# Optimization experiments

Hardware: AMD Instinct MI355X
Metric: run time of the kernel (lower is better)

## Reference

```python
import jax, jax.numpy as jnp
import numpy as np

N_QUBITS = 20
W_MUL = (2.0 ** 0.5) * (5.0 ** -0.5)  # he_std = gain * 5**-0.5, use_wscale=True, lrmul=1

_C = jnp.complex64
X = jnp.array([[0, 1], [1, 0]], dtype=_C)
Y = jnp.array([[0, -1j], [1j, 0]], dtype=_C)
Z = jnp.array([[1, 0], [0, -1]], dtype=_C)
I2 = jnp.eye(2, dtype=_C)
I4 = jnp.eye(4, dtype=_C)
XX = jnp.kron(X, X)
YY = jnp.kron(Y, Y)
ZZ = jnp.kron(Z, Z)


def _rot(theta, pauli, ident):
    # exp(-i * theta/2 * P) = cos(theta/2) I - i sin(theta/2) P
    a = theta * 0.5
    return jnp.cos(a) * ident - (1j * jnp.sin(a)) * pauli


def _apply_1q(state, g, w):
    # state: [batch] + [2]*n ; contract gate input index with qubit axis w
    s = jnp.tensordot(g, state, axes=((1,), (w + 1,)))
    return jnp.moveaxis(s, 0, w + 1)


def _apply_2q(state, g4, w0, w1):
    g = g4.reshape(2, 2, 2, 2)  # (out0, out1, in0, in1)
    s = jnp.tensordot(g, state, axes=((2, 3), (w0 + 1, w1 + 1)))
    return jnp.moveaxis(s, (0, 1), (w0 + 1, w1 + 1))


def _xyz_layer(psi, params, n):
    # params: [3n]; rx, ry, rz on each wire
    for q in range(n):
        psi = _apply_1q(psi, _rot(params[3 * q], X, I2), q)
        psi = _apply_1q(psi, _rot(params[3 * q + 1], Y, I2), q)
        psi = _apply_1q(psi, _rot(params[3 * q + 2], Z, I2), q)
    return psi


def _circuit(psi, w, n):
    psi = _xyz_layer(psi, w[: 3 * n], n)
    for q in range(n - 1):
        i = 3 * n + 3 * q
        psi = _apply_2q(psi, _rot(w[i], XX, I4), q, q + 1)
        psi = _apply_2q(psi, _rot(w[i + 1], YY, I4), q, q + 1)
        psi = _apply_2q(psi, _rot(w[i + 2], ZZ, I4), q, q + 1)
    psi = _xyz_layer(psi, w[6 * n - 3 :], n)
    return psi


def setup_inputs() -> dict:
    key = jax.random.key(0)
    k1, k2 = jax.random.split(key)
    n = N_QUBITS
    dim = 1 << n
    batch = 4
    x = jax.random.normal(k1, (batch, 1, dim), dtype=jnp.float32)
    weight = jax.random.uniform(k2, (9 * n - 3,), dtype=jnp.float32, minval=0.0, maxval=2.0 * np.pi)
    return {"x": x, "weight": weight, "dimA": 10}


def reference(x, weight, dimA):
    n = N_QUBITS
    batch = x.shape[0]
    w = weight * W_MUL
    psi = x.astype(_C).reshape((batch,) + (2,) * n)  # MPS tensor [b, 2, ..., 2]
    psi = _circuit(psi, w, n)
    dimB = n - dimA
    # partial trace of |psi><psi| over the first dimB qubits (most-significant axes):
    # reduced[a, c] = sum_t psi[t, a] * conj(psi[t, c])  -- never materialize the full DM
    psi = psi.reshape(batch, 1 << dimB, 1 << dimA)
    rdm = jnp.einsum('bta,btc->bac', psi, psi.conj())
    # return real/imag stacked on last axis (real-valued representation of complex DM)
    return jnp.stack([rdm.real, rdm.imag], axis=-1)
```

## Files before the change

### kernel.cpp

```cpp
#include <hip/hip_runtime.h>
#include <hip/hip_bf16.h>

#define N_Q    20
#define DIM    (1 << N_Q)
#define BATCH  4
#define NGATES 19
#define L2OFF  117
#define GSTRIDE 32

typedef float2 c32;
typedef __attribute__((ext_vector_type(2))) float fv2;
typedef __attribute__((ext_vector_type(8))) short short8;
typedef __attribute__((ext_vector_type(4))) float f32x4;
typedef __attribute__((ext_vector_type(4))) unsigned int u32x4;

__device__ __forceinline__ c32 cmul(c32 a, c32 b) {
    return make_float2(fmaf(a.x, b.x, -a.y * b.y), fmaf(a.x, b.y, a.y * b.x));
}
__device__ __forceinline__ c32 cmadd(c32 acc, c32 a, c32 b) {
    acc.x = fmaf(a.x, b.x, fmaf(-a.y, b.y, acc.x));
    acc.y = fmaf(a.x, b.y, fmaf(a.y, b.x, acc.y));
    return acc;
}
__device__ __forceinline__ unsigned short f2bf(float f) {
    union { float f; unsigned u; } v; v.f = f;
    unsigned r = v.u + 0x7FFFu + ((v.u >> 16) & 1u);
    return (unsigned short)(r >> 16);
}
__device__ __forceinline__ unsigned pack_bf2(float re, float im) {
    return (unsigned)f2bf(re) | ((unsigned)f2bf(im) << 16);
}
__device__ __forceinline__ fv2 unpack_bf2(unsigned w) {
    union { unsigned u; float f; } lo, hi;
    lo.u = (w & 0xFFFFu) << 16;
    hi.u = w & 0xFFFF0000u;
    return (fv2){lo.f, hi.f};
}
__device__ __forceinline__ void gll16(const void* g, void* l) {
    __builtin_amdgcn_global_load_lds((const __attribute__((address_space(1))) void*)g,
                                     (__attribute__((address_space(3))) void*)l, 16, 0, 0);
}

__device__ void mm2(const c32 A[2][2], const c32 B[2][2], c32 C[2][2]) {
    for (int i = 0; i < 2; i++)
        for (int j = 0; j < 2; j++) {
            c32 s = make_float2(0.f, 0.f);
            for (int k = 0; k < 2; k++) s = cmadd(s, A[i][k], B[k][j]);
            C[i][j] = s;
        }
}
__device__ void mm4(const c32 A[4][4], const c32 B[4][4], c32 C[4][4]) {
    for (int i = 0; i < 4; i++)
        for (int j = 0; j < 4; j++) {
            c32 s = make_float2(0.f, 0.f);
            for (int k = 0; k < 4; k++) s = cmadd(s, A[i][k], B[k][j]);
            C[i][j] = s;
        }
}
__device__ void single_u(const float* w, int base, c32 U[2][2]) {
    const float WM = 0.63245553203367586640f;
    float hx = w[base] * WM * 0.5f, hy = w[base + 1] * WM * 0.5f, hz = w[base + 2] * WM * 0.5f;
    float cx = cosf(hx), sx = sinf(hx);
    float cy = cosf(hy), sy = sinf(hy);
    float cz = cosf(hz), sz = sinf(hz);
    c32 RX[2][2] = {{{cx, 0.f}, {0.f, -sx}}, {{0.f, -sx}, {cx, 0.f}}};
    c32 RY[2][2] = {{{cy, 0.f}, {-sy, 0.f}}, {{sy, 0.f}, {cy, 0.f}}};
    c32 RZ[2][2] = {{{cz, -sz}, {0.f, 0.f}}, {{0.f, 0.f}, {cz, sz}}};
    c32 T[2][2];
    mm2(RY, RX, T);
    mm2(RZ, T, U);
}
__device__ void kron22(const c32 A[2][2], const c32 B[2][2], c32 K[4][4]) {
    for (int i = 0; i < 2; i++)
        for (int j = 0; j < 2; j++)
            for (int k = 0; k < 2; k++)
                for (int l = 0; l < 2; l++)
                    K[i * 2 + j][k * 2 + l] = cmul(A[i][k], B[j][l]);
}

__global__ void build_gates(const float* __restrict__ w, c32* __restrict__ G) {
    int q = threadIdx.x;
    if (q >= NGATES) return;
    const float WM = 0.63245553203367586640f;
    float hx = w[60 + 3 * q] * WM * 0.5f;
    float hy = w[61 + 3 * q] * WM * 0.5f;
    float hz = w[62 + 3 * q] * WM * 0.5f;
    float cx = cosf(hx), sx = sinf(hx);
    float cy = cosf(hy), sy = sinf(hy);
    float cz = cosf(hz), sz = sinf(hz);
    c32 RXX[4][4], RYY[4][4], RZZ[4][4];
    for (int i = 0; i < 4; i++)
        for (int j = 0; j < 4; j++) {
            RXX[i][j] = make_float2(0.f, 0.f);
            RYY[i][j] = make_float2(0.f, 0.f);
            RZZ[i][j] = make_float2(0.f, 0.f);
        }
    for (int i = 0; i < 4; i++) {
        RXX[i][i]     = make_float2(cx, 0.f);
        RXX[i][3 - i] = make_float2(0.f, -sx);
        RYY[i][i]     = make_float2(cy, 0.f);
    }
    RYY[0][3] = make_float2(0.f,  sy);
    RYY[1][2] = make_float2(0.f, -sy);
    RYY[2][1] = make_float2(0.f, -sy);
    RYY[3][0] = make_float2(0.f,  sy);
    RZZ[0][0] = make_float2(cz, -sz);
    RZZ[1][1] = make_float2(cz,  sz);
    RZZ[2][2] = make_float2(cz,  sz);
    RZZ[3][3] = make_float2(cz, -sz);
    c32 T[4][4], M[4][4];
    mm4(RYY, RXX, T);
    mm4(RZZ, T, M);

    c32 I2m[2][2] = {{{1.f, 0.f}, {0.f, 0.f}}, {{0.f, 0.f}, {1.f, 0.f}}};
    c32 Ua[2][2], Ub[2][2], Pre[4][4], Post[4][4];
    if (q == 0) {
        single_u(w, 0, Ua);
        single_u(w, 3, Ub);
        kron22(Ua, Ub, Pre);
    } else {
        single_u(w, 3 * (q + 1), Ub);
        kron22(I2m, Ub, Pre);
    }
    if (q == NGATES - 1) {
        single_u(w, L2OFF + 3 * 18, Ua);
        single_u(w, L2OFF + 3 * 19, Ub);
        kron22(Ua, Ub, Post);
    } else {
        single_u(w, L2OFF + 3 * q, Ua);
        kron22(Ua, I2m, Post);
    }
    c32 T2[4][4], Gq[4][4];
    mm4(M, Pre, T2);
    mm4(Post, T2, Gq);
    for (int i = 0; i < 4; i++)
        for (int j = 0; j < 4; j++) {
            c32 g = Gq[i][j];
            G[q * GSTRIDE + i * 4 + j]      = g;
            G[q * GSTRIDE + 16 + i * 4 + j] = make_float2(-g.y, g.x);
        }
}

__device__ __forceinline__ void apply4pk(const fv2 g[16], const fv2 gs[16],
                                         fv2& x0, fv2& x1, fv2& x2, fv2& x3) {
    fv2 a0 = (fv2)(x0[0]), b0 = (fv2)(x0[1]);
    fv2 a1 = (fv2)(x1[0]), b1 = (fv2)(x1[1]);
    fv2 a2 = (fv2)(x2[0]), b2 = (fv2)(x2[1]);
    fv2 a3 = (fv2)(x3[0]), b3 = (fv2)(x3[1]);
    fv2 r0 = a0 * g[0];  r0 += b0 * gs[0];  r0 += a1 * g[1];  r0 += b1 * gs[1];
    r0 += a2 * g[2];     r0 += b2 * gs[2];  r0 += a3 * g[3];  r0 += b3 * gs[3];
    fv2 r1 = a0 * g[4];  r1 += b0 * gs[4];  r1 += a1 * g[5];  r1 += b1 * gs[5];
    r1 += a2 * g[6];     r1 += b2 * gs[6];  r1 += a3 * g[7];  r1 += b3 * gs[7];
    fv2 r2 = a0 * g[8];  r2 += b0 * gs[8];  r2 += a1 * g[9];  r2 += b1 * gs[9];
    r2 += a2 * g[10];    r2 += b2 * gs[10]; r2 += a3 * g[11]; r2 += b3 * gs[11];
    fv2 r3 = a0 * g[12]; r3 += b0 * gs[12]; r3 += a1 * g[13]; r3 += b1 * gs[13];
    r3 += a2 * g[14];    r3 += b2 * gs[14]; r3 += a3 * g[15]; r3 += b3 * gs[15];
    x0 = r0; x1 = r1; x2 = r2; x3 = r3;
}
__device__ __forceinline__ void load_gate2(const fv2* __restrict__ gp, fv2 g[16], fv2 gs[16]) {
#pragma unroll
    for (int k = 0; k < 16; k++) { g[k] = gp[k]; gs[k] = gp[16 + k]; }
}
template <int LO>
__device__ __forceinline__ void gate_on32(fv2 v[32], const fv2 g[16], const fv2 gs[16]) {
#pragma unroll
    for (int m = 0; m < 8; ++m) {
        const int j0 = ((m >> LO) << (LO + 2)) | (m & ((1 << LO) - 1));
        const int s = 1 << LO;
        apply4pk(g, gs, v[j0], v[j0 + s], v[j0 + 2 * s], v[j0 + 3 * s]);
    }
}
template <int LO>
__device__ __forceinline__ void gate_on16(fv2* v, const fv2 g[16], const fv2 gs[16]) {
#pragma unroll
    for (int m = 0; m < 4; ++m) {
        const int j0 = ((m >> LO) << (LO + 2)) | (m & ((1 << LO) - 1));
        const int s = 1 << LO;
        apply4pk(g, gs, v[j0], v[j0 + s], v[j0 + 2 * s], v[j0 + 3 * s]);
    }
}

#define SIDX(l) ((l) ^ ((((l) >> 5) & 15)))

__global__ __launch_bounds__(256) void pass_a2(const float* __restrict__ x,
                                               unsigned* __restrict__ psiB,
                                               const c32* __restrict__ Gall) {
    __shared__ __align__(16) char smem[65536];
    float* xs = (float*)smem;
    fv2* s = (fv2*)smem;
    const fv2* Gf = (const fv2*)Gall;
    int b = blockIdx.x >> 7;
    int c0 = (blockIdx.x & 127) << 5;
    const float* xp = x + ((size_t)b << 20) + c0;
    unsigned* ppb = psiB + ((size_t)b << 20) + c0;
    int t = threadIdx.x;
#pragma unroll
    for (int i = 0; i < 8; ++i) {
        int f4 = t + (i << 8);
        int row = f4 >> 3, sl = f4 & 7;
        float4 v = *reinterpret_cast<const float4*>(xp + (size_t)row * 4096 + sl * 4);
        reinterpret_cast<float4*>(xs)[row * 8 + (sl ^ (row & 7))] = v;
    }
    __syncthreads();
    int col = t & 31, rlow = t >> 5;
    fv2 v[32], g[16], gs[16];
#pragma unroll
    for (int j = 0; j < 32; ++j) {
        int row = (j << 3) | rlow;
        float re = xs[row * 32 + ((((col >> 2) ^ (row & 7)) << 2) | (col & 3))];
        v[j] = (fv2){re, 0.f};
    }
    __syncthreads();
    load_gate2(Gf + 0 * GSTRIDE, g, gs);  gate_on32<3>(v, g, gs);
    load_gate2(Gf + 1 * GSTRIDE, g, gs);  gate_on32<2>(v, g, gs);
    load_gate2(Gf + 2 * GSTRIDE, g, gs);  gate_on32<1>(v, g, gs);
    load_gate2(Gf + 3 * GSTRIDE, g, gs);  gate_on32<0>(v, g, gs);
#pragma unroll
    for (int j = 0; j < 32; ++j) {
        int l = ((((j << 3) | rlow) << 5)) | col;
        s[SIDX(l)] = v[j];
    }
    __syncthreads();
    int rhi = t >> 5;
#pragma unroll
    for (int rtop = 0; rtop < 2; ++rtop)
#pragma unroll
        for (int j = 0; j < 16; ++j) {
            int row = (rtop << 7) | (rhi << 4) | j;
            int l = (row << 5) | col;
            v[rtop * 16 + j] = s[SIDX(l)];
        }
    load_gate2(Gf + 4 * GSTRIDE, g, gs);  gate_on16<2>(v, g, gs);  gate_on16<2>(v + 16, g, gs);
    load_gate2(Gf + 5 * GSTRIDE, g, gs);  gate_on16<1>(v, g, gs);  gate_on16<1>(v + 16, g, gs);
    load_gate2(Gf + 6 * GSTRIDE, g, gs);  gate_on16<0>(v, g, gs);  gate_on16<0>(v + 16, g, gs);
#pragma unroll
    for (int rtop = 0; rtop < 2; ++rtop)
#pragma unroll
        for (int j = 0; j < 16; ++j) {
            int row = (rtop << 7) | (rhi << 4) | j;
            fv2 val = v[rtop * 16 + j];
            ppb[(size_t)row * 4096 + col] = pack_bf2(val[0], val[1]);
        }
}

__global__ __launch_bounds__(256) void pass_b2(const unsigned* __restrict__ psiB,
                                               unsigned short* __restrict__ Brt,
                                               unsigned short* __restrict__ Bit,
                                               const c32* __restrict__ Gall) {
    __shared__ fv2 s[8192];
    const fv2* Gf = (const fv2*)Gall;
    int b = blockIdx.x >> 7;
    int chunk = blockIdx.x & 127;
    const unsigned* ppb = psiB + ((size_t)b << 20) + ((size_t)chunk << 13);
    int t = threadIdx.x;
    fv2 v[32], g[16], gs[16];
#pragma unroll
    for (int j = 0; j < 32; ++j) v[j] = unpack_bf2(ppb[(j << 8) | t]);
    load_gate2(Gf + 7 * GSTRIDE, g, gs);   gate_on32<3>(v, g, gs);
    load_gate2(Gf + 8 * GSTRIDE, g, gs);   gate_on32<2>(v, g, gs);
    load_gate2(Gf + 9 * GSTRIDE, g, gs);   gate_on32<1>(v, g, gs);
    load_gate2(Gf + 10 * GSTRIDE, g, gs);  gate_on32<0>(v, g, gs);
#pragma unroll
    for (int j = 0; j < 32; ++j) { int l = (j << 8) | t; s[SIDX(l)] = v[j]; }
    __syncthreads();
    int hi2 = (t >> 4) << 9, lo2 = t & 15;
#pragma unroll
    for (int j = 0; j < 32; ++j) { int l = hi2 | (j << 4) | lo2; v[j] = s[SIDX(l)]; }
    load_gate2(Gf + 11 * GSTRIDE, g, gs);  gate_on32<3>(v, g, gs);
    load_gate2(Gf + 12 * GSTRIDE, g, gs);  gate_on32<2>(v, g, gs);
    load_gate2(Gf + 13 * GSTRIDE, g, gs);  gate_on32<1>(v, g, gs);
    load_gate2(Gf + 14 * GSTRIDE, g, gs);  gate_on32<0>(v, g, gs);
    __syncthreads();
#pragma unroll
    for (int j = 0; j < 32; ++j) { int l = hi2 | (j << 4) | lo2; s[SIDX(l)] = v[j]; }
    __syncthreads();
#pragma unroll
    for (int j = 0; j < 32; ++j) { int l = (t << 5) | j; v[j] = s[SIDX(l)]; }
    load_gate2(Gf + 15 * GSTRIDE, g, gs);  gate_on32<3>(v, g, gs);
    load_gate2(Gf + 16 * GSTRIDE, g, gs);  gate_on32<2>(v, g, gs);
    load_gate2(Gf + 17 * GSTRIDE, g, gs);  gate_on32<1>(v, g, gs);
    load_gate2(Gf + 18 * GSTRIDE, g, gs);  gate_on32<0>(v, g, gs);
    size_t off = ((size_t)b << 20) + ((size_t)chunk << 13) + ((size_t)t << 5);
#pragma unroll
    for (int p = 0; p < 4; ++p) {
        unsigned short rr[8], ri[8];
#pragma unroll
        for (int i = 0; i < 8; ++i) {
            rr[i] = f2bf(v[8 * p + i][0]);
            ri[i] = f2bf(v[8 * p + i][1]);
        }
        *reinterpret_cast<float4*>(Brt + off + 8 * p) = *reinterpret_cast<float4*>(rr);
        *reinterpret_cast<float4*>(Bit + off + 8 * p) = *reinterpret_cast<float4*>(ri);
    }
}

__global__ __launch_bounds__(256) void bt_t(const unsigned short* __restrict__ Brt,
                                            const unsigned short* __restrict__ Bit,
                                            unsigned short* __restrict__ Art,
                                            unsigned short* __restrict__ Ait) {
    __shared__ unsigned lds32[64 * 66];
    int b  = blockIdx.z;
    int t0 = blockIdx.x * 64;
    int a0 = blockIdx.y * 64;
    size_t gb = (size_t)b << 20;
#pragma unroll
    for (int h = 0; h < 2; ++h) {
        int p = threadIdx.x + h * 256;
        int r = p >> 3, cq = p & 7;
        size_t src = gb + (size_t)(t0 + r) * 1024 + a0 + cq * 8;
        float4 fr = *reinterpret_cast<const float4*>(Brt + src);
        float4 fi = *reinterpret_cast<const float4*>(Bit + src);
        const unsigned short* ur = reinterpret_cast<const unsigned short*>(&fr);
        const unsigned short* ui = reinterpret_cast<const unsigned short*>(&fi);
#pragma unroll
        for (int i = 0; i < 8; ++i)
            lds32[r * 66 + cq * 8 + i] = (unsigned)ur[i] | ((unsigned)ui[i] << 16);
    }
    __syncthreads();
#pragma unroll
    for (int h = 0; h < 2; ++h) {
        int q = threadIdx.x + h * 256;
        int a = q >> 3, tq = q & 7;
        unsigned short rr[8], ri[8];
#pragma unroll
        for (int i = 0; i < 8; ++i) {
            unsigned w = lds32[(tq * 8 + i) * 66 + a];
            rr[i] = (unsigned short)(w & 0xFFFF);
            ri[i] = (unsigned short)(w >> 16);
        }
        size_t dst = gb + (size_t)(a0 + a) * 1024 + t0 + tq * 8;
        *reinterpret_cast<float4*>(Art + dst) = *reinterpret_cast<float4*>(rr);
        *reinterpret_cast<float4*>(Ait + dst) = *reinterpret_cast<float4*>(ri);
    }
}

__global__ __launch_bounds__(512) void gram_mfma5c(const unsigned short* __restrict__ Art,
                                                   const unsigned short* __restrict__ Ait,
                                                   float2* __restrict__ out) {
    __shared__ __align__(16) unsigned short lds[2][4][8192];
    int hw = blockIdx.x;
    int virt = (hw & 7) * 18 + (hw >> 3);
    int b = virt / 36;
    int rem = virt - b * 36;
    int ia = 0;
    while (rem >= 8 - ia) { rem -= 8 - ia; ++ia; }
    int ic = ia + rem;
    int a0 = ia * 128, c0 = ic * 128;
    int tid = threadIdx.x;
    int lane = tid & 63, w = tid >> 6;
    int wm = w & 3, wn = w >> 2;
    int arr = w >> 1, half = w & 1;
    const unsigned short* sp = (arr & 1) ? Ait : Art;
    int prow = (arr < 2) ? a0 : c0;
    int srow = lane >> 3, sslot = lane & 7;
    size_t gb = (size_t)b << 20;

    f32x4 accRe[2][4], accIm[2][4];
#pragma unroll
    for (int m = 0; m < 2; m++)
#pragma unroll
        for (int n = 0; n < 4; n++) { accRe[m][n] = (f32x4)0.f; accIm[m][n] = (f32x4)0.f; }

#define STAGE5(KT, BUF)                                                                   \
    {                                                                                     \
        _Pragma("unroll")                                                                 \
        for (int i = 0; i < 8; ++i) {                                                     \
            int r = (half << 6) | (i << 3) | srow;                                        \
            int sl = sslot ^ srow;                                                        \
            const unsigned short* gp = sp + gb + ((size_t)(prow + r) << 10) + (KT) * 64 + sl * 8; \
            gll16(gp, &lds[BUF][arr][((half << 6) | (i << 3)) * 64 + lane * 8]);          \
        }                                                                                 \
    }

    STAGE5(0, 0);
    for (int kt = 0; kt < 16; ++kt) {
        int cur = kt & 1;
        asm volatile("s_waitcnt vmcnt(0)" ::: "memory");
        __builtin_amdgcn_s_barrier();
        __builtin_amdgcn_sched_barrier(0);
        if (kt < 15) STAGE5(kt + 1, cur ^ 1);
        __builtin_amdgcn_s_setprio(1);
#pragma unroll
        for (int kk = 0; kk < 2; ++kk) {
            int sbase = kk * 4 + (lane >> 4);
            short8 am[2][2], bn[4][2];
#pragma unroll
            for (int m = 0; m < 2; m++) {
                int r = wm * 32 + m * 16 + (lane & 15);
                int off = r * 64 + ((sbase ^ (r & 7)) << 3);
                am[m][0] = *reinterpret_cast<const short8*>(&lds[cur][0][off]);
                am[m][1] = *reinterpret_cast<const short8*>(&lds[cur][1][off]);
            }
#pragma unroll
            for (int n = 0; n < 4; n++) {
                int r = wn * 64 + n * 16 + (lane & 15);
                int off = r * 64 + ((sbase ^ (r & 7)) << 3);
                bn[n][0] = *reinterpret_cast<const short8*>(&lds[cur][2][off]);
                bn[n][1] = *reinterpret_cast<const short8*>(&lds[cur][3][off]);
            }
#pragma unroll
            for (int m = 0; m < 2; m++) {
                u32x4 tn = *reinterpret_cast<u32x4*>(&am[m][0]) ^ 0x80008000u;
                short8 arn = *reinterpret_cast<short8*>(&tn);
#pragma unroll
                for (int n = 0; n < 4; n++) {
                    accRe[m][n] = __builtin_amdgcn_mfma_f32_16x16x32_bf16(am[m][0], bn[n][0], accRe[m][n], 0, 0, 0);
                    accRe[m][n] = __builtin_amdgcn_mfma_f32_16x16x32_bf16(am[m][1], bn[n][1], accRe[m][n], 0, 0, 0);
                    accIm[m][n] = __builtin_amdgcn_mfma_f32_16x16x32_bf16(am[m][1], bn[n][0], accIm[m][n], 0, 0, 0);
                    accIm[m][n] = __builtin_amdgcn_mfma_f32_16x16x32_bf16(arn,      bn[n][1], accIm[m][n], 0, 0, 0);
                }
            }
        }
        __builtin_amdgcn_s_setprio(0);
        asm volatile("s_waitcnt lgkmcnt(0)" ::: "memory");
        __builtin_amdgcn_sched_barrier(0);
    }
#undef STAGE5
    size_t ob = gb;
#pragma unroll
    for (int m = 0; m < 2; m++)
#pragma unroll
        for (int n = 0; n < 4; n++)
#pragma unroll
            for (int r = 0; r < 4; r++) {
                int a = a0 + wm * 32 + m * 16 + (lane >> 4) * 4 + r;
                int c = c0 + wn * 64 + n * 16 + (lane & 15);
                out[ob + ((size_t)a << 10) + c] = make_float2(accRe[m][n][r], accIm[m][n][r]);
            }
    if (ia != ic) {
        float2* mlds = reinterpret_cast<float2*>(&lds[0][0][0]);
#pragma unroll
        for (int h = 0; h < 2; ++h) {
            __syncthreads();
            if (wn == h) {
#pragma unroll
                for (int m = 0; m < 2; m++)
#pragma unroll
                    for (int n = 0; n < 4; n++)
#pragma unroll
                        for (int r = 0; r < 4; r++) {
                            int a_l = wm * 32 + m * 16 + (lane >> 4) * 4 + r;
                            int c_l = n * 16 + (lane & 15);
                            mlds[c_l * 131 + a_l] = make_float2(accRe[m][n][r], -accIm[m][n][r]);
                        }
            }
            __syncthreads();
#pragma unroll
            for (int i = 0; i < 16; ++i) {
                int p = tid + (i << 9);
                int row = p >> 7, col = p & 127;
                out[ob + ((size_t)(c0 + h * 64 + row) << 10) + a0 + col] = mlds[row * 131 + col];
            }
        }
    }
}

extern "C" void kernel_launch(void* const* d_in, const int* in_sizes, int n_in,
                              void* d_out, int out_size, void* d_ws, size_t ws_size,
                              hipStream_t stream) {
    const float* x = (const float*)d_in[0];
    const float* weight = (const float*)d_in[1];
    const size_t psiBytes = (size_t)BATCH * DIM * sizeof(unsigned);
    unsigned* psiB = (unsigned*)d_ws;
    c32* G = (c32*)((char*)d_ws + psiBytes);
    unsigned short* Brt = (unsigned short*)((char*)d_ws + psiBytes + 65536);
    unsigned short* Bit = Brt + (size_t)BATCH * DIM;
    unsigned short* Art = Bit + (size_t)BATCH * DIM;
    unsigned short* Ait = Art + (size_t)BATCH * DIM;

    build_gates<<<1, 64, 0, stream>>>(weight, G);
    pass_a2<<<BATCH * 128, 256, 0, stream>>>(x, psiB, G);
    pass_b2<<<BATCH * 128, 256, 0, stream>>>(psiB, Brt, Bit, G);
    bt_t<<<dim3(16, 16, BATCH), 256, 0, stream>>>(Brt, Bit, Art, Ait);
    gram_mfma5c<<<144, 512, 0, stream>>>(Art, Ait, (float2*)d_out);
}
```

Measured before the change: 94.38 us.

## Fuse transpose into pass_b2 epilogue and drop separate bt_t kernel

The final transpose that built the a-major bf16 planes is folded into pass_b2: after the last gate stage, each block stages its 8 t-rows by 1024 a-columns chunk in LDS with an XOR swizzle and writes 16-byte segments directly into the transposed Art/Ait layout. This removes one kernel launch and a full global round trip of the intermediate bf16 buffers. In exchange, the writes are now 16-byte pieces strided by 2 KB per row, which may coalesce less well, and pass_b2 gains an extra LDS pass and barrier.

```diff
diff --git a/kernel.cpp b/kernel.cpp
--- a/kernel.cpp
+++ b/kernel.cpp
@@ -181,6 +181,7 @@
 }
 
 #define SIDX(l) ((l) ^ ((((l) >> 5) & 15)))
+#define TIDX(a, tl) (((a) << 3) | ((tl) ^ (((a) >> 5) & 7)))
 
 __global__ __launch_bounds__(256) void pass_a2(const float* __restrict__ x,
                                                unsigned* __restrict__ psiB,
@@ -244,8 +245,8 @@
 }
 
 __global__ __launch_bounds__(256) void pass_b2(const unsigned* __restrict__ psiB,
-                                               unsigned short* __restrict__ Brt,
-                                               unsigned short* __restrict__ Bit,
+                                               unsigned short* __restrict__ Art,
+                                               unsigned short* __restrict__ Ait,
                                                const c32* __restrict__ Gall) {
     __shared__ fv2 s[8192];
     const fv2* Gf = (const fv2*)Gall;
@@ -280,57 +281,34 @@
     load_gate2(Gf + 16 * GSTRIDE, g, gs);  gate_on32<2>(v, g, gs);
     load_gate2(Gf + 17 * GSTRIDE, g, gs);  gate_on32<1>(v, g, gs);
     load_gate2(Gf + 18 * GSTRIDE, g, gs);  gate_on32<0>(v, g, gs);
-    size_t off = ((size_t)b << 20) + ((size_t)chunk << 13) + ((size_t)t << 5);
-#pragma unroll
-    for (int p = 0; p < 4; ++p) {
-        unsigned short rr[8], ri[8];
-#pragma unroll
-        for (int i = 0; i < 8; ++i) {
-            rr[i] = f2bf(v[8 * p + i][0]);
-            ri[i] = f2bf(v[8 * p + i][1]);
-        }
-        *reinterpret_cast<float4*>(Brt + off + 8 * p) = *reinterpret_cast<float4*>(rr);
-        *reinterpret_cast<float4*>(Bit + off + 8 * p) = *reinterpret_cast<float4*>(ri);
-    }
-}
-
-__global__ __launch_bounds__(256) void bt_t(const unsigned short* __restrict__ Brt,
-                                            const unsigned short* __restrict__ Bit,
-                                            unsigned short* __restrict__ Art,
-                                            unsigned short* __restrict__ Ait) {
-    __shared__ unsigned lds32[64 * 66];
-    int b  = blockIdx.z;
-    int t0 = blockIdx.x * 64;
-    int a0 = blockIdx.y * 64;
-    size_t gb = (size_t)b << 20;
-#pragma unroll
-    for (int h = 0; h < 2; ++h) {
-        int p = threadIdx.x + h * 256;
-        int r = p >> 3, cq = p & 7;
-        size_t src = gb + (size_t)(t0 + r) * 1024 + a0 + cq * 8;
-        float4 fr = *reinterpret_cast<const float4*>(Brt + src);
-        float4 fi = *reinterpret_cast<const float4*>(Bit + src);
-        const unsigned short* ur = reinterpret_cast<const unsigned short*>(&fr);
-        const unsigned short* ui = reinterpret_cast<const unsigned short*>(&fi);
-#pragma unroll
-        for (int i = 0; i < 8; ++i)
-            lds32[r * 66 + cq * 8 + i] = (unsigned)ur[i] | ((unsigned)ui[i] << 16);
-    }
-    __syncthreads();
-#pragma unroll
-    for (int h = 0; h < 2; ++h) {
-        int q = threadIdx.x + h * 256;
-        int a = q >> 3, tq = q & 7;
-        unsigned short rr[8], ri[8];
-#pragma unroll
-        for (int i = 0; i < 8; ++i) {
-            unsigned w = lds32[(tq * 8 + i) * 66 + a];
-            rr[i] = (unsigned short)(w & 0xFFFF);
-            ri[i] = (unsigned short)(w >> 16);
-        }
-        size_t dst = gb + (size_t)(a0 + a) * 1024 + t0 + tq * 8;
-        *reinterpret_cast<float4*>(Art + dst) = *reinterpret_cast<float4*>(rr);
-        *reinterpret_cast<float4*>(Ait + dst) = *reinterpret_cast<float4*>(ri);
+    __syncthreads();
+    {
+        int tlw = t >> 5;
+        int abase = (t & 31) << 5;
+#pragma unroll
+        for (int j = 0; j < 32; ++j) {
+            int a = abase + j;
+            s[TIDX(a, tlw)] = v[j];
+        }
+    }
+    __syncthreads();
+    {
+        int w = t >> 6, lane = t & 63;
+        size_t gb = (size_t)b << 20;
+#pragma unroll
+        for (int i = 0; i < 4; ++i) {
+            int a = (w << 8) | (i << 6) | lane;
+            unsigned short rr[8], ri[8];
+#pragma unroll
+            for (int tl = 0; tl < 8; ++tl) {
+                fv2 q = s[TIDX(a, tl)];
+                rr[tl] = f2bf(q[0]);
+                ri[tl] = f2bf(q[1]);
+            }
+            size_t dst = gb + ((size_t)a << 10) + (chunk << 3);
+            *reinterpret_cast<float4*>(Art + dst) = *reinterpret_cast<float4*>(rr);
+            *reinterpret_cast<float4*>(Ait + dst) = *reinterpret_cast<float4*>(ri);
+        }
     }
 }
 
@@ -463,14 +441,11 @@
     const size_t psiBytes = (size_t)BATCH * DIM * sizeof(unsigned);
     unsigned* psiB = (unsigned*)d_ws;
     c32* G = (c32*)((char*)d_ws + psiBytes);
-    unsigned short* Brt = (unsigned short*)((char*)d_ws + psiBytes + 65536);
-    unsigned short* Bit = Brt + (size_t)BATCH * DIM;
-    unsigned short* Art = Bit + (size_t)BATCH * DIM;
+    unsigned short* Art = (unsigned short*)((char*)d_ws + psiBytes + 65536);
     unsigned short* Ait = Art + (size_t)BATCH * DIM;
 
     build_gates<<<1, 64, 0, stream>>>(weight, G);
     pass_a2<<<BATCH * 128, 256, 0, stream>>>(x, psiB, G);
-    pass_b2<<<BATCH * 128, 256, 0, stream>>>(psiB, Brt, Bit, G);
-    bt_t<<<dim3(16, 16, BATCH), 256, 0, stream>>>(Brt, Bit, Art, Ait);
+    pass_b2<<<BATCH * 128, 256, 0, stream>>>(psiB, Art, Ait, G);
     gram_mfma5c<<<144, 512, 0, stream>>>(Art, Ait, (float2*)d_out);
 }
```

After: 93.70 us, median of 2. No clear change (-0.7%).
